# Kernel tuning notes

Hardware: AMD Instinct MI355X
Metric: run time of the kernel (lower is better)

The kernel has to match this reference:

```python
import jax, jax.numpy as jnp
import numpy as np

N_NODES = 50000
D_FEAT = 128
N_EDGES_1 = 800_000
N_EDGES_2 = 2_400_000


def setup_inputs() -> dict:
    key = jax.random.key(0)
    k = jax.random.split(key, 7)
    x = jax.random.normal(k[0], (N_NODES, D_FEAT), dtype=jnp.float32)
    row1 = jax.random.randint(k[1], (N_EDGES_1,), 0, N_NODES, dtype=jnp.int32)
    col1 = jax.random.randint(k[2], (N_EDGES_1,), 0, N_NODES, dtype=jnp.int32)
    vals1 = jax.random.uniform(k[3], (N_EDGES_1,), dtype=jnp.float32)
    row2 = jax.random.randint(k[4], (N_EDGES_2,), 0, N_NODES, dtype=jnp.int32)
    col2 = jax.random.randint(k[5], (N_EDGES_2,), 0, N_NODES, dtype=jnp.int32)
    vals2 = jax.random.uniform(k[6], (N_EDGES_2,), dtype=jnp.float32)
    return {"x": x, "row1": row1, "col1": col1, "vals1": vals1,
            "row2": row2, "col2": col2, "vals2": vals2}


def _spmm(row, col, vals, x, n_nodes):
    # (A @ x)[i] = sum_{e: row[e]==i} vals[e] * x[col[e]]
    msgs = vals[:, None] * x[col]          # [E, d] gathered, weighted messages
    return jax.ops.segment_sum(msgs, row, num_segments=n_nodes)  # [N, d]


def reference(x, row1, col1, vals1, row2, col2, vals2):
    x1 = _spmm(row1, col1, vals1, x, N_NODES)   # 1-hop aggregation
    x2 = _spmm(row2, col2, vals2, x, N_NODES)   # 2-hop aggregation
    return jnp.concatenate([x1, x2], axis=1)    # [N, 2d]
```

## Files before the change

kernel.cpp:

```cpp
#include <hip/hip_runtime.h>


constexpr int D = 128;
constexpr int OUT_STRIDE = 256;
constexpr int NBMAX = 800;
constexpr int BATCH = 4096;
constexpr int LRECS = 3840;

struct KP {
  const float* x;
  const int* row1; const int* col1; const float* vals1;
  const int* row2; const int* col2; const float* vals2;
  float* out;
  int n, e1, e2, nx4, nb, cap1, cap2, t1, ntasks;
  int* gcur;
  unsigned short* xb;
  uint2* seg1;
  uint2* seg2;
};

__device__ __forceinline__ unsigned short f2b(float f) {
  unsigned u = __float_as_uint(f);
  u += 0x7fffu + ((u >> 16) & 1u);
  return (unsigned short)(u >> 16);
}
__device__ __forceinline__ float blo(unsigned u) { return __uint_as_float(u << 16); }
__device__ __forceinline__ float bhi(unsigned u) { return __uint_as_float(u & 0xffff0000u); }

__launch_bounds__(256)
__global__ void cvt_zero_k(KP p) {
  const int i = blockIdx.x * 256 + threadIdx.x;
  const int GT = gridDim.x * 256;
  for (int j = i; j < 2 * p.nb; j += GT) p.gcur[j] = 0;
  for (int j = i; j < p.nx4; j += GT) {
    const float4 v = ((const float4*)p.x)[j];
    ushort4 o; o.x = f2b(v.x); o.y = f2b(v.y); o.z = f2b(v.z); o.w = f2b(v.w);
    ((ushort4*)p.xb)[j] = o;
  }
}

__launch_bounds__(256)
__global__ void bucket_scatter_k(KP p) {
  __shared__ uint2 srecs[BATCH];
  __shared__ int cnts[NBMAX];
  __shared__ int lstart[NBMAX];
  __shared__ int curs[NBMAX];
  __shared__ int gbase[NBMAX];
  __shared__ int wsum[4];
  const int tid  = threadIdx.x;
  const int lane = tid & 63;
  const int wid  = tid >> 6;
  const int nb   = p.nb;

  const int task  = blockIdx.x;
  const int hop   = (task >= p.t1);
  const int tbase = (hop ? (task - p.t1) : task) * BATCH;
  const int E     = hop ? p.e2 : p.e1;
  const int m     = min(BATCH, E - tbase);
  const int* rowp = hop ? p.row2 : p.row1;
  const int* colp = hop ? p.col2 : p.col1;
  const float* vp = hop ? p.vals2 : p.vals1;
  const int cap   = hop ? p.cap2 : p.cap1;
  uint2* seg      = hop ? p.seg2 : p.seg1;
  int* gc         = p.gcur + (hop ? nb : 0);

  for (int b = tid; b < NBMAX; b += 256) cnts[b] = 0;
  __syncthreads();

  #pragma unroll
  for (int k = 0; k < BATCH / 1024; ++k) {
    const int i4 = tid + k * 256;
    const int e0 = i4 * 4;
    if (e0 < m) {
      if (e0 + 3 < m) {
        const int4 r = ((const int4*)(rowp + tbase))[i4];
        atomicAdd(&cnts[r.x >> 6], 1);
        atomicAdd(&cnts[r.y >> 6], 1);
        atomicAdd(&cnts[r.z >> 6], 1);
        atomicAdd(&cnts[r.w >> 6], 1);
      } else {
        for (int j = e0; j < m; ++j) atomicAdd(&cnts[rowp[tbase + j] >> 6], 1);
      }
    }
  }
  __syncthreads();

  int c0 = 0, c1 = 0, c2 = 0, c3 = 0, s = 0;
  const int b0 = tid * 4;
  if (b0 < NBMAX) {
    c0 = cnts[b0]; c1 = cnts[b0 + 1]; c2 = cnts[b0 + 2]; c3 = cnts[b0 + 3];
    s = c0 + c1 + c2 + c3;
  }
  int acc = s;
  #pragma unroll
  for (int d = 1; d < 64; d <<= 1) { int t = __shfl_up(acc, d); if (lane >= d) acc += t; }
  if (lane == 63) wsum[wid] = acc;
  __syncthreads();
  int woff = 0;
  #pragma unroll
  for (int w = 0; w < 4; ++w) if (w < wid) woff += wsum[w];
  if (b0 < NBMAX) {
    const int ex = woff + acc - s;
    lstart[b0]     = ex;                curs[b0]     = ex;
    lstart[b0 + 1] = ex + c0;           curs[b0 + 1] = ex + c0;
    lstart[b0 + 2] = ex + c0 + c1;      curs[b0 + 2] = ex + c0 + c1;
    lstart[b0 + 3] = ex + c0 + c1 + c2; curs[b0 + 3] = ex + c0 + c1 + c2;
  }

  for (int i = tid; i < nb; i += 256) {
    const int b = (i + task * 37) % nb;
    const int c = cnts[b];
    gbase[b] = c ? atomicAdd(&gc[b], c) : 0;
  }
  __syncthreads();

  #pragma unroll
  for (int k = 0; k < BATCH / 1024; ++k) {
    const int i4 = tid + k * 256;
    const int e0 = i4 * 4;
    if (e0 < m) {
      if (e0 + 3 < m) {
        const int4  rr = ((const int4*)(rowp + tbase))[i4];
        const int4  cc = ((const int4*)(colp + tbase))[i4];
        const float4 vv = ((const float4*)(vp + tbase))[i4];
        {
          const int r = rr.x, b = r >> 6;
          const unsigned meta = (unsigned)cc.x | ((unsigned)(r & 63) << 16) | ((unsigned)b << 22);
          srecs[atomicAdd(&curs[b], 1)] = make_uint2(meta, __float_as_uint(vv.x));
        }
        {
          const int r = rr.y, b = r >> 6;
          const unsigned meta = (unsigned)cc.y | ((unsigned)(r & 63) << 16) | ((unsigned)b << 22);
          srecs[atomicAdd(&curs[b], 1)] = make_uint2(meta, __float_as_uint(vv.y));
        }
        {
          const int r = rr.z, b = r >> 6;
          const unsigned meta = (unsigned)cc.z | ((unsigned)(r & 63) << 16) | ((unsigned)b << 22);
          srecs[atomicAdd(&curs[b], 1)] = make_uint2(meta, __float_as_uint(vv.z));
        }
        {
          const int r = rr.w, b = r >> 6;
          const unsigned meta = (unsigned)cc.w | ((unsigned)(r & 63) << 16) | ((unsigned)b << 22);
          srecs[atomicAdd(&curs[b], 1)] = make_uint2(meta, __float_as_uint(vv.w));
        }
      } else {
        for (int j = e0; j < m; ++j) {
          const int r = rowp[tbase + j], b = r >> 6;
          const unsigned meta = (unsigned)colp[tbase + j] | ((unsigned)(r & 63) << 16) | ((unsigned)b << 22);
          srecs[atomicAdd(&curs[b], 1)] = make_uint2(meta, __float_as_uint(vp[tbase + j]));
        }
      }
    }
  }
  __syncthreads();

  for (int t = tid; t < m; t += 256) {
    const uint2 rec = srecs[t];
    const int b = rec.x >> 22;
    const int pos = gbase[b] + (t - lstart[b]);
    if (pos < cap) seg[(size_t)b * cap + pos] = rec;
  }
}

__launch_bounds__(256)
__global__ void sort_gather_k(KP p) {
  __shared__ uint2 lrecs[LRECS];
  __shared__ int rstart[65];
  __shared__ int lcur[64];
  const int tid  = threadIdx.x;
  const int lane = tid & 63;
  const int wid  = tid >> 6;
  const int nb   = p.nb;
  const int hop  = (blockIdx.x < nb) ? 1 : 0;
  const int b    = hop ? blockIdx.x : blockIdx.x - nb;
  const int cap  = hop ? p.cap2 : p.cap1;
  const uint2* seg = (hop ? p.seg2 : p.seg1) + (size_t)b * cap;
  const int cnt  = min(p.gcur[(hop ? nb : 0) + b], cap);
  const uint4* xq = (const uint4*)p.xb;

  if (tid < 64) lcur[tid] = 0;
  __syncthreads();
  for (int t = tid; t < cnt; t += 256)
    atomicAdd(&lcur[(seg[t].x >> 16) & 63u], 1);
  __syncthreads();

  if (tid < 64) {
    const int c = lcur[tid];
    int acc = c;
    #pragma unroll
    for (int d = 1; d < 64; d <<= 1) { int t = __shfl_up(acc, d); if (lane >= d) acc += t; }
    const int ex = acc - c;
    rstart[tid] = ex;
    lcur[tid] = ex;
    if (tid == 63) rstart[64] = acc;
  }
  __syncthreads();

  for (int t = tid; t < cnt; t += 256) {
    const uint2 rec = seg[t];
    const int rl = (int)((rec.x >> 16) & 63u);
    const int pos = atomicAdd(&lcur[rl], 1);
    lrecs[pos] = rec;
  }
  __syncthreads();

  const int g   = lane >> 4;
  const int sub = lane & 15;
  const int rbase = b * 64;

  for (int r = wid; r < 64; r += 4) {
    const int rg = rbase + r;
    if (rg >= p.n) break;
    const int start = rstart[r];
    const int end   = rstart[r + 1];
    float a0 = 0.f, a1 = 0.f, a2 = 0.f, a3 = 0.f;
    float a4 = 0.f, a5 = 0.f, a6 = 0.f, a7 = 0.f;
    if (end > start) {
      int idx = start + g;
      uint2 qA = lrecs[idx < end ? idx : end - 1];
      float vA = (idx < end) ? __uint_as_float(qA.y) : 0.f;
      uint4 xA = xq[(qA.x & 0xffffu) * 16u + (unsigned)sub];

      for (int j = start + 4; j < end; j += 4) {
        idx = j + g;
        const uint2 qB = lrecs[idx < end ? idx : end - 1];
        const float vB = (idx < end) ? __uint_as_float(qB.y) : 0.f;
        const uint4 xB = xq[(qB.x & 0xffffu) * 16u + (unsigned)sub];

        a0 = fmaf(vA, blo(xA.x), a0); a1 = fmaf(vA, bhi(xA.x), a1);
        a2 = fmaf(vA, blo(xA.y), a2); a3 = fmaf(vA, bhi(xA.y), a3);
        a4 = fmaf(vA, blo(xA.z), a4); a5 = fmaf(vA, bhi(xA.z), a5);
        a6 = fmaf(vA, blo(xA.w), a6); a7 = fmaf(vA, bhi(xA.w), a7);

        vA = vB; xA = xB;
      }
      a0 = fmaf(vA, blo(xA.x), a0); a1 = fmaf(vA, bhi(xA.x), a1);
      a2 = fmaf(vA, blo(xA.y), a2); a3 = fmaf(vA, bhi(xA.y), a3);
      a4 = fmaf(vA, blo(xA.z), a4); a5 = fmaf(vA, bhi(xA.z), a5);
      a6 = fmaf(vA, blo(xA.w), a6); a7 = fmaf(vA, bhi(xA.w), a7);

      a0 += __shfl_xor(a0, 16); a0 += __shfl_xor(a0, 32);
      a1 += __shfl_xor(a1, 16); a1 += __shfl_xor(a1, 32);
      a2 += __shfl_xor(a2, 16); a2 += __shfl_xor(a2, 32);
      a3 += __shfl_xor(a3, 16); a3 += __shfl_xor(a3, 32);
      a4 += __shfl_xor(a4, 16); a4 += __shfl_xor(a4, 32);
      a5 += __shfl_xor(a5, 16); a5 += __shfl_xor(a5, 32);
      a6 += __shfl_xor(a6, 16); a6 += __shfl_xor(a6, 32);
      a7 += __shfl_xor(a7, 16); a7 += __shfl_xor(a7, 32);
    }
    if (g == 0) {
      float* op = p.out + (size_t)rg * OUT_STRIDE + hop * D + sub * 8;
      ((float4*)op)[0] = make_float4(a0, a1, a2, a3);
      ((float4*)op)[1] = make_float4(a4, a5, a6, a7);
    }
  }
}

extern "C" void kernel_launch(void* const* d_in, const int* in_sizes, int n_in,
                              void* d_out, int out_size, void* d_ws, size_t ws_size,
                              hipStream_t stream) {
  KP p;
  p.x     = (const float*)d_in[0];
  p.row1  = (const int*)  d_in[1];
  p.col1  = (const int*)  d_in[2];
  p.vals1 = (const float*)d_in[3];
  p.row2  = (const int*)  d_in[4];
  p.col2  = (const int*)  d_in[5];
  p.vals2 = (const float*)d_in[6];
  p.out   = (float*)d_out;

  p.e1  = in_sizes[1];
  p.e2  = in_sizes[4];
  p.n   = out_size / OUT_STRIDE;
  p.nx4 = in_sizes[0] / 4;
  p.nb  = (p.n + 63) >> 6;
  if (p.nb > NBMAX || p.n > 65535) return;

  {
    const float m1 = (float)p.e1 / p.nb, m2 = (float)p.e2 / p.nb;
    p.cap1 = ((int)(m1 + 10.f * __builtin_sqrtf(m1) + 64.f) + 7) & ~7;
    p.cap2 = ((int)(m2 + 10.f * __builtin_sqrtf(m2) + 64.f) + 7) & ~7;
    if (p.cap1 > LRECS) p.cap1 = LRECS;
    if (p.cap2 > LRECS) p.cap2 = LRECS;
  }
  p.t1     = (p.e1 + BATCH - 1) / BATCH;
  p.ntasks = p.t1 + (p.e2 + BATCH - 1) / BATCH;

  char* w = (char*)d_ws;
  size_t off = 0;
  p.gcur = (int*)w;                       off += (size_t)(2 * p.nb) * 4;
  off = (off + 15) & ~(size_t)15;
  p.xb   = (unsigned short*)(w + off);    off += (size_t)in_sizes[0] * 2;
  off = (off + 15) & ~(size_t)15;
  p.seg1 = (uint2*)(w + off);             off += (size_t)p.nb * p.cap1 * 8;
  p.seg2 = (uint2*)(w + off);             off += (size_t)p.nb * p.cap2 * 8;
  if (ws_size < off) return;

  cvt_zero_k      <<<1024,      256, 0, stream>>>(p);
  bucket_scatter_k<<<p.ntasks,  256, 0, stream>>>(p);
  sort_gather_k   <<<2 * p.nb,  256, 0, stream>>>(p);
}
```

Baseline: 275.5 us.

## Split bf16 features into column quarters and run persistent gather blocks per quarter

The bf16 copy of x is stored as four column-quarter planes of 32 features each. The gather kernel becomes a persistent grid of 512 blocks with 512 threads, split between the two hops in proportion to their edge counts. Each block walks its row buckets once per quarter, so the gathered working set per pass is a quarter of x, which may fit better in cache. In exchange, every bucket is re-sorted four times, there are more barriers, and each load is narrower (8 bytes instead of 16).

```diff
diff --git a/kernel.cpp b/kernel.cpp
--- a/kernel.cpp
+++ b/kernel.cpp
@@ -12,7 +12,7 @@
   const int* row1; const int* col1; const float* vals1;
   const int* row2; const int* col2; const float* vals2;
   float* out;
-  int n, e1, e2, nx4, nb, cap1, cap2, t1, ntasks;
+  int n, e1, e2, nx4, nb, cap1, cap2, t1, ntasks, g1, g2;
   int* gcur;
   unsigned short* xb;
   uint2* seg1;
@@ -35,7 +35,11 @@
   for (int j = i; j < p.nx4; j += GT) {
     const float4 v = ((const float4*)p.x)[j];
     ushort4 o; o.x = f2b(v.x); o.y = f2b(v.y); o.z = f2b(v.z); o.w = f2b(v.w);
-    ((ushort4*)p.xb)[j] = o;
+    const int node = j >> 5;
+    const int f4   = j & 31;
+    const int q    = f4 >> 3;
+    const int k    = f4 & 7;
+    ((ushort4*)p.xb)[((size_t)q * p.n + node) * 8 + k] = o;
   }
 }
 
@@ -162,7 +166,7 @@
   }
 }
 
-__launch_bounds__(256)
+__launch_bounds__(512)
 __global__ void sort_gather_k(KP p) {
   __shared__ uint2 lrecs[LRECS];
   __shared__ int rstart[65];
@@ -170,88 +174,101 @@
   const int tid  = threadIdx.x;
   const int lane = tid & 63;
   const int wid  = tid >> 6;
+  const int g    = lane >> 3;
+  const int sub  = lane & 7;
   const int nb   = p.nb;
-  const int hop  = (blockIdx.x < nb) ? 1 : 0;
-  const int b    = hop ? blockIdx.x : blockIdx.x - nb;
-  const int cap  = hop ? p.cap2 : p.cap1;
-  const uint2* seg = (hop ? p.seg2 : p.seg1) + (size_t)b * cap;
-  const int cnt  = min(p.gcur[(hop ? nb : 0) + b], cap);
-  const uint4* xq = (const uint4*)p.xb;
-
-  if (tid < 64) lcur[tid] = 0;
-  __syncthreads();
-  for (int t = tid; t < cnt; t += 256)
-    atomicAdd(&lcur[(seg[t].x >> 16) & 63u], 1);
-  __syncthreads();
-
-  if (tid < 64) {
-    const int c = lcur[tid];
-    int acc = c;
-    #pragma unroll
-    for (int d = 1; d < 64; d <<= 1) { int t = __shfl_up(acc, d); if (lane >= d) acc += t; }
-    const int ex = acc - c;
-    rstart[tid] = ex;
-    lcur[tid] = ex;
-    if (tid == 63) rstart[64] = acc;
-  }
-  __syncthreads();
-
-  for (int t = tid; t < cnt; t += 256) {
-    const uint2 rec = seg[t];
-    const int rl = (int)((rec.x >> 16) & 63u);
-    const int pos = atomicAdd(&lcur[rl], 1);
-    lrecs[pos] = rec;
-  }
-  __syncthreads();
-
-  const int g   = lane >> 4;
-  const int sub = lane & 15;
-  const int rbase = b * 64;
-
-  for (int r = wid; r < 64; r += 4) {
-    const int rg = rbase + r;
-    if (rg >= p.n) break;
-    const int start = rstart[r];
-    const int end   = rstart[r + 1];
-    float a0 = 0.f, a1 = 0.f, a2 = 0.f, a3 = 0.f;
-    float a4 = 0.f, a5 = 0.f, a6 = 0.f, a7 = 0.f;
-    if (end > start) {
-      int idx = start + g;
-      uint2 qA = lrecs[idx < end ? idx : end - 1];
-      float vA = (idx < end) ? __uint_as_float(qA.y) : 0.f;
-      uint4 xA = xq[(qA.x & 0xffffu) * 16u + (unsigned)sub];
-
-      for (int j = start + 4; j < end; j += 4) {
-        idx = j + g;
-        const uint2 qB = lrecs[idx < end ? idx : end - 1];
-        const float vB = (idx < end) ? __uint_as_float(qB.y) : 0.f;
-        const uint4 xB = xq[(qB.x & 0xffffu) * 16u + (unsigned)sub];
-
-        a0 = fmaf(vA, blo(xA.x), a0); a1 = fmaf(vA, bhi(xA.x), a1);
-        a2 = fmaf(vA, blo(xA.y), a2); a3 = fmaf(vA, bhi(xA.y), a3);
-        a4 = fmaf(vA, blo(xA.z), a4); a5 = fmaf(vA, bhi(xA.z), a5);
-        a6 = fmaf(vA, blo(xA.w), a6); a7 = fmaf(vA, bhi(xA.w), a7);
-
-        vA = vB; xA = xB;
-      }
-      a0 = fmaf(vA, blo(xA.x), a0); a1 = fmaf(vA, bhi(xA.x), a1);
-      a2 = fmaf(vA, blo(xA.y), a2); a3 = fmaf(vA, bhi(xA.y), a3);
-      a4 = fmaf(vA, blo(xA.z), a4); a5 = fmaf(vA, bhi(xA.z), a5);
-      a6 = fmaf(vA, blo(xA.w), a6); a7 = fmaf(vA, bhi(xA.w), a7);
-
-      a0 += __shfl_xor(a0, 16); a0 += __shfl_xor(a0, 32);
-      a1 += __shfl_xor(a1, 16); a1 += __shfl_xor(a1, 32);
-      a2 += __shfl_xor(a2, 16); a2 += __shfl_xor(a2, 32);
-      a3 += __shfl_xor(a3, 16); a3 += __shfl_xor(a3, 32);
-      a4 += __shfl_xor(a4, 16); a4 += __shfl_xor(a4, 32);
-      a5 += __shfl_xor(a5, 16); a5 += __shfl_xor(a5, 32);
-      a6 += __shfl_xor(a6, 16); a6 += __shfl_xor(a6, 32);
-      a7 += __shfl_xor(a7, 16); a7 += __shfl_xor(a7, 32);
-    }
-    if (g == 0) {
-      float* op = p.out + (size_t)rg * OUT_STRIDE + hop * D + sub * 8;
-      ((float4*)op)[0] = make_float4(a0, a1, a2, a3);
-      ((float4*)op)[1] = make_float4(a4, a5, a6, a7);
+
+  const int hop = (blockIdx.x < p.g2) ? 1 : 0;
+  const int s   = hop ? blockIdx.x : (blockIdx.x - p.g2);
+  const int gs  = hop ? p.g2 : p.g1;
+  const int b_lo = (int)((long long)s * nb / gs);
+  const int b_hi = (int)((long long)(s + 1) * nb / gs);
+  const int cap = hop ? p.cap2 : p.cap1;
+  const uint2* segh = hop ? p.seg2 : p.seg1;
+  const int* gch = p.gcur + (hop ? nb : 0);
+
+  for (int q = 0; q < 4; ++q) {
+    const uint2* xq = (const uint2*)(p.xb + (size_t)q * p.n * 32);
+    for (int b = b_lo; b < b_hi; ++b) {
+      const uint2* seg = segh + (size_t)b * cap;
+      const int cnt = min(gch[b], cap);
+
+      uint2 rr0, rr1, rr2, rr3, rr4, rr5, rr6, rr7;
+      if (tid < 64) lcur[tid] = 0;
+      __syncthreads();
+      {
+        int t = tid;
+        if (t < cnt) { rr0 = seg[t]; atomicAdd(&lcur[(rr0.x >> 16) & 63u], 1); } t += 512;
+        if (t < cnt) { rr1 = seg[t]; atomicAdd(&lcur[(rr1.x >> 16) & 63u], 1); } t += 512;
+        if (t < cnt) { rr2 = seg[t]; atomicAdd(&lcur[(rr2.x >> 16) & 63u], 1); } t += 512;
+        if (t < cnt) { rr3 = seg[t]; atomicAdd(&lcur[(rr3.x >> 16) & 63u], 1); } t += 512;
+        if (t < cnt) { rr4 = seg[t]; atomicAdd(&lcur[(rr4.x >> 16) & 63u], 1); } t += 512;
+        if (t < cnt) { rr5 = seg[t]; atomicAdd(&lcur[(rr5.x >> 16) & 63u], 1); } t += 512;
+        if (t < cnt) { rr6 = seg[t]; atomicAdd(&lcur[(rr6.x >> 16) & 63u], 1); } t += 512;
+        if (t < cnt) { rr7 = seg[t]; atomicAdd(&lcur[(rr7.x >> 16) & 63u], 1); }
+      }
+      __syncthreads();
+
+      if (tid < 64) {
+        const int c = lcur[tid];
+        int acc = c;
+        #pragma unroll
+        for (int d = 1; d < 64; d <<= 1) { int t = __shfl_up(acc, d); if (lane >= d) acc += t; }
+        const int ex = acc - c;
+        rstart[tid] = ex;
+        lcur[tid] = ex;
+        if (tid == 63) rstart[64] = acc;
+      }
+      __syncthreads();
+
+      {
+        int t = tid;
+        if (t < cnt) lrecs[atomicAdd(&lcur[(rr0.x >> 16) & 63u], 1)] = rr0; t += 512;
+        if (t < cnt) lrecs[atomicAdd(&lcur[(rr1.x >> 16) & 63u], 1)] = rr1; t += 512;
+        if (t < cnt) lrecs[atomicAdd(&lcur[(rr2.x >> 16) & 63u], 1)] = rr2; t += 512;
+        if (t < cnt) lrecs[atomicAdd(&lcur[(rr3.x >> 16) & 63u], 1)] = rr3; t += 512;
+        if (t < cnt) lrecs[atomicAdd(&lcur[(rr4.x >> 16) & 63u], 1)] = rr4; t += 512;
+        if (t < cnt) lrecs[atomicAdd(&lcur[(rr5.x >> 16) & 63u], 1)] = rr5; t += 512;
+        if (t < cnt) lrecs[atomicAdd(&lcur[(rr6.x >> 16) & 63u], 1)] = rr6; t += 512;
+        if (t < cnt) lrecs[atomicAdd(&lcur[(rr7.x >> 16) & 63u], 1)] = rr7;
+      }
+      __syncthreads();
+
+      const int rbase = b * 64;
+      #pragma unroll
+      for (int i = 0; i < 8; ++i) {
+        const int r  = wid + (i << 3);
+        const int rg = rbase + r;
+        const int rs = rstart[r];
+        const int re = rstart[r + 1];
+        float a0 = 0.f, a1 = 0.f, a2 = 0.f, a3 = 0.f;
+        if (re > rs) {
+          int idx = rs + g;
+          uint2 qA = lrecs[idx < re ? idx : re - 1];
+          float vA = (idx < re) ? __uint_as_float(qA.y) : 0.f;
+          uint2 xA = xq[(qA.x & 0xffffu) * 8u + (unsigned)sub];
+          for (int t8 = rs + 8; t8 < re; t8 += 8) {
+            idx = t8 + g;
+            const uint2 qB = lrecs[idx < re ? idx : re - 1];
+            const float vB = (idx < re) ? __uint_as_float(qB.y) : 0.f;
+            const uint2 xB = xq[(qB.x & 0xffffu) * 8u + (unsigned)sub];
+            a0 = fmaf(vA, blo(xA.x), a0); a1 = fmaf(vA, bhi(xA.x), a1);
+            a2 = fmaf(vA, blo(xA.y), a2); a3 = fmaf(vA, bhi(xA.y), a3);
+            vA = vB; xA = xB;
+          }
+          a0 = fmaf(vA, blo(xA.x), a0); a1 = fmaf(vA, bhi(xA.x), a1);
+          a2 = fmaf(vA, blo(xA.y), a2); a3 = fmaf(vA, bhi(xA.y), a3);
+          a0 += __shfl_xor(a0, 8); a0 += __shfl_xor(a0, 16); a0 += __shfl_xor(a0, 32);
+          a1 += __shfl_xor(a1, 8); a1 += __shfl_xor(a1, 16); a1 += __shfl_xor(a1, 32);
+          a2 += __shfl_xor(a2, 8); a2 += __shfl_xor(a2, 16); a2 += __shfl_xor(a2, 32);
+          a3 += __shfl_xor(a3, 8); a3 += __shfl_xor(a3, 16); a3 += __shfl_xor(a3, 32);
+        }
+        if (g == 0 && rg < p.n) {
+          float* op = p.out + (size_t)rg * OUT_STRIDE + hop * D + q * 32 + sub * 4;
+          *((float4*)op) = make_float4(a0, a1, a2, a3);
+        }
+      }
+      __syncthreads();
     }
   }
 }
@@ -286,6 +303,15 @@
   p.t1     = (p.e1 + BATCH - 1) / BATCH;
   p.ntasks = p.t1 + (p.e2 + BATCH - 1) / BATCH;
 
+  {
+    const long long et = (long long)p.e1 + p.e2;
+    int g2 = (int)((512LL * p.e2 + et / 2) / et);
+    if (g2 < 1) g2 = 1;
+    if (g2 > 511) g2 = 511;
+    p.g2 = g2;
+    p.g1 = 512 - g2;
+  }
+
   char* w = (char*)d_ws;
   size_t off = 0;
   p.gcur = (int*)w;                       off += (size_t)(2 * p.nb) * 4;
@@ -298,5 +324,5 @@
 
   cvt_zero_k      <<<1024,      256, 0, stream>>>(p);
   bucket_scatter_k<<<p.ntasks,  256, 0, stream>>>(p);
-  sort_gather_k   <<<2 * p.nb,  256, 0, stream>>>(p);
-}
+  sort_gather_k   <<<512,       512, 0, stream>>>(p);
+}
```

After: 451.7 us. 1.64x slower.

## Replace global atomic bucket reservation with count/scan/scatter passes and deepen gather pipeline

Applied to the files above, without the earlier changes.

Splits the bucket scatter into a per-task count kernel, a column-wise scan over tasks, and a scatter kernel that reads precomputed base offsets, replacing global atomicAdd reservations. The scatter output becomes deterministic and global atomic contention goes away. The cost is two extra launches, a second read of row indices, and a serial scan run by only 2 blocks over roughly 780 tasks per bucket. The gather loop also keeps four loads in flight instead of one to hide memory latency, at the cost of more registers.

```diff
diff --git a/kernel.cpp b/kernel.cpp
--- a/kernel.cpp
+++ b/kernel.cpp
@@ -14,6 +14,8 @@
   float* out;
   int n, e1, e2, nx4, nb, cap1, cap2, t1, ntasks;
   int* gcur;
+  int* counts;
+  int* base;
   unsigned short* xb;
   uint2* seg1;
   uint2* seg2;
@@ -28,10 +30,9 @@
 __device__ __forceinline__ float bhi(unsigned u) { return __uint_as_float(u & 0xffff0000u); }
 
 __launch_bounds__(256)
-__global__ void cvt_zero_k(KP p) {
+__global__ void cvt_k(KP p) {
   const int i = blockIdx.x * 256 + threadIdx.x;
   const int GT = gridDim.x * 256;
-  for (int j = i; j < 2 * p.nb; j += GT) p.gcur[j] = 0;
   for (int j = i; j < p.nx4; j += GT) {
     const float4 v = ((const float4*)p.x)[j];
     ushort4 o; o.x = f2b(v.x); o.y = f2b(v.y); o.z = f2b(v.z); o.w = f2b(v.w);
@@ -40,29 +41,16 @@
 }
 
 __launch_bounds__(256)
-__global__ void bucket_scatter_k(KP p) {
-  __shared__ uint2 srecs[BATCH];
+__global__ void count_k(KP p) {
   __shared__ int cnts[NBMAX];
-  __shared__ int lstart[NBMAX];
-  __shared__ int curs[NBMAX];
-  __shared__ int gbase[NBMAX];
-  __shared__ int wsum[4];
-  const int tid  = threadIdx.x;
-  const int lane = tid & 63;
-  const int wid  = tid >> 6;
-  const int nb   = p.nb;
-
+  const int tid = threadIdx.x;
+  const int nb  = p.nb;
   const int task  = blockIdx.x;
   const int hop   = (task >= p.t1);
   const int tbase = (hop ? (task - p.t1) : task) * BATCH;
   const int E     = hop ? p.e2 : p.e1;
   const int m     = min(BATCH, E - tbase);
   const int* rowp = hop ? p.row2 : p.row1;
-  const int* colp = hop ? p.col2 : p.col1;
-  const float* vp = hop ? p.vals2 : p.vals1;
-  const int cap   = hop ? p.cap2 : p.cap1;
-  uint2* seg      = hop ? p.seg2 : p.seg1;
-  int* gc         = p.gcur + (hop ? nb : 0);
 
   for (int b = tid; b < NBMAX; b += 256) cnts[b] = 0;
   __syncthreads();
@@ -85,6 +73,58 @@
   }
   __syncthreads();
 
+  int* crow = p.counts + (size_t)task * nb;
+  for (int b = tid; b < nb; b += 256) crow[b] = cnts[b];
+}
+
+__launch_bounds__(1024)
+__global__ void scan_k(KP p) {
+  const int hop = blockIdx.x;
+  const int t0  = hop ? p.t1 : 0;
+  const int te  = hop ? p.ntasks : p.t1;
+  const int nb  = p.nb;
+  for (int b = threadIdx.x; b < nb; b += 1024) {
+    int acc = 0;
+    for (int t = t0; t < te; ++t) {
+      const size_t idx = (size_t)t * nb + b;
+      const int c = p.counts[idx];
+      p.base[idx] = acc;
+      acc += c;
+    }
+    p.gcur[hop * nb + b] = acc;
+  }
+}
+
+__launch_bounds__(256)
+__global__ void scatter_k(KP p) {
+  __shared__ uint2 srecs[BATCH];
+  __shared__ int lstart[NBMAX];
+  __shared__ int curs[NBMAX];
+  __shared__ int gbase[NBMAX];
+  __shared__ int wsum[4];
+  const int tid  = threadIdx.x;
+  const int lane = tid & 63;
+  const int wid  = tid >> 6;
+  const int nb   = p.nb;
+
+  const int task  = blockIdx.x;
+  const int hop   = (task >= p.t1);
+  const int tbase = (hop ? (task - p.t1) : task) * BATCH;
+  const int E     = hop ? p.e2 : p.e1;
+  const int m     = min(BATCH, E - tbase);
+  const int* rowp = hop ? p.row2 : p.row1;
+  const int* colp = hop ? p.col2 : p.col1;
+  const float* vp = hop ? p.vals2 : p.vals1;
+  const int cap   = hop ? p.cap2 : p.cap1;
+  uint2* seg      = hop ? p.seg2 : p.seg1;
+  const int* brow = p.base   + (size_t)task * nb;
+  const int* crow = p.counts + (size_t)task * nb;
+
+  __shared__ int cnts[NBMAX];
+  for (int b = tid; b < nb; b += 256) { gbase[b] = brow[b]; cnts[b] = crow[b]; }
+  for (int b = nb + tid; b < NBMAX; b += 256) cnts[b] = 0;
+  __syncthreads();
+
   int c0 = 0, c1 = 0, c2 = 0, c3 = 0, s = 0;
   const int b0 = tid * 4;
   if (b0 < NBMAX) {
@@ -105,12 +145,6 @@
     lstart[b0 + 1] = ex + c0;           curs[b0 + 1] = ex + c0;
     lstart[b0 + 2] = ex + c0 + c1;      curs[b0 + 2] = ex + c0 + c1;
     lstart[b0 + 3] = ex + c0 + c1 + c2; curs[b0 + 3] = ex + c0 + c1 + c2;
-  }
-
-  for (int i = tid; i < nb; i += 256) {
-    const int b = (i + task * 37) % nb;
-    const int c = cnts[b];
-    gbase[b] = c ? atomicAdd(&gc[b], c) : 0;
   }
   __syncthreads();
 
@@ -211,33 +245,35 @@
   for (int r = wid; r < 64; r += 4) {
     const int rg = rbase + r;
     if (rg >= p.n) break;
-    const int start = rstart[r];
-    const int end   = rstart[r + 1];
+    const int rs = rstart[r];
+    const int re = rstart[r + 1];
     float a0 = 0.f, a1 = 0.f, a2 = 0.f, a3 = 0.f;
     float a4 = 0.f, a5 = 0.f, a6 = 0.f, a7 = 0.f;
-    if (end > start) {
-      int idx = start + g;
-      uint2 qA = lrecs[idx < end ? idx : end - 1];
-      float vA = (idx < end) ? __uint_as_float(qA.y) : 0.f;
-      uint4 xA = xq[(qA.x & 0xffffu) * 16u + (unsigned)sub];
-
-      for (int j = start + 4; j < end; j += 4) {
-        idx = j + g;
-        const uint2 qB = lrecs[idx < end ? idx : end - 1];
-        const float vB = (idx < end) ? __uint_as_float(qB.y) : 0.f;
-        const uint4 xB = xq[(qB.x & 0xffffu) * 16u + (unsigned)sub];
-
-        a0 = fmaf(vA, blo(xA.x), a0); a1 = fmaf(vA, bhi(xA.x), a1);
-        a2 = fmaf(vA, blo(xA.y), a2); a3 = fmaf(vA, bhi(xA.y), a3);
-        a4 = fmaf(vA, blo(xA.z), a4); a5 = fmaf(vA, bhi(xA.z), a5);
-        a6 = fmaf(vA, blo(xA.w), a6); a7 = fmaf(vA, bhi(xA.w), a7);
-
-        vA = vB; xA = xB;
+    if (re > rs) {
+      auto LD = [&](int idx, float& v, uint4& xv) {
+        const uint2 q = lrecs[idx < re ? idx : re - 1];
+        v = (idx < re) ? __uint_as_float(q.y) : 0.f;
+        xv = xq[(q.x & 0xffffu) * 16u + (unsigned)sub];
+      };
+      #define FMA_G(v, xv)                                            \
+        a0 = fmaf(v, blo(xv.x), a0); a1 = fmaf(v, bhi(xv.x), a1);     \
+        a2 = fmaf(v, blo(xv.y), a2); a3 = fmaf(v, bhi(xv.y), a3);     \
+        a4 = fmaf(v, blo(xv.z), a4); a5 = fmaf(v, bhi(xv.z), a5);     \
+        a6 = fmaf(v, blo(xv.w), a6); a7 = fmaf(v, bhi(xv.w), a7);
+
+      float v0, v1, v2, v3; uint4 x0, x1, x2, x3;
+      const int j0 = rs + g;
+      LD(j0, v0, x0); LD(j0 + 4, v1, x1); LD(j0 + 8, v2, x2); LD(j0 + 12, v3, x3);
+      const int iters = (re - rs + 15) >> 4;
+      for (int it = 1; it < iters; ++it) {
+        const int jn = j0 + (it << 4);
+        FMA_G(v0, x0); LD(jn,      v0, x0);
+        FMA_G(v1, x1); LD(jn + 4,  v1, x1);
+        FMA_G(v2, x2); LD(jn + 8,  v2, x2);
+        FMA_G(v3, x3); LD(jn + 12, v3, x3);
       }
-      a0 = fmaf(vA, blo(xA.x), a0); a1 = fmaf(vA, bhi(xA.x), a1);
-      a2 = fmaf(vA, blo(xA.y), a2); a3 = fmaf(vA, bhi(xA.y), a3);
-      a4 = fmaf(vA, blo(xA.z), a4); a5 = fmaf(vA, bhi(xA.z), a5);
-      a6 = fmaf(vA, blo(xA.w), a6); a7 = fmaf(vA, bhi(xA.w), a7);
+      FMA_G(v0, x0); FMA_G(v1, x1); FMA_G(v2, x2); FMA_G(v3, x3);
+      #undef FMA_G
 
       a0 += __shfl_xor(a0, 16); a0 += __shfl_xor(a0, 32);
       a1 += __shfl_xor(a1, 16); a1 += __shfl_xor(a1, 32);
@@ -294,9 +330,15 @@
   off = (off + 15) & ~(size_t)15;
   p.seg1 = (uint2*)(w + off);             off += (size_t)p.nb * p.cap1 * 8;
   p.seg2 = (uint2*)(w + off);             off += (size_t)p.nb * p.cap2 * 8;
+  off = (off + 15) & ~(size_t)15;
+  p.counts = (int*)(w + off);             off += (size_t)p.ntasks * p.nb * 4;
+  off = (off + 15) & ~(size_t)15;
+  p.base = (int*)(w + off);               off += (size_t)p.ntasks * p.nb * 4;
   if (ws_size < off) return;
 
-  cvt_zero_k      <<<1024,      256, 0, stream>>>(p);
-  bucket_scatter_k<<<p.ntasks,  256, 0, stream>>>(p);
-  sort_gather_k   <<<2 * p.nb,  256, 0, stream>>>(p);
-}
+  cvt_k     <<<1024,      256, 0, stream>>>(p);
+  count_k   <<<p.ntasks,  256, 0, stream>>>(p);
+  scan_k    <<<2,        1024, 0, stream>>>(p);
+  scatter_k <<<p.ntasks,  256, 0, stream>>>(p);
+  sort_gather_k<<<2 * p.nb, 256, 0, stream>>>(p);
+}
```

Measured after the change: 412.3 us. 49.6% more time.
